# Kernel tuning notes

Hardware: AMD Instinct MI355X
Metric: run time of the kernel (lower is better)

## Reference

```python
import jax, jax.numpy as jnp
import numpy as np

E, D_MODEL, D_HIDDEN, TOK_PER_EXP = 64, 1024, 4096, 128


def setup_inputs() -> dict:
    key = jax.random.key(0)
    k1, k2, k3 = jax.random.split(key, 3)
    n_tokens = E * TOK_PER_EXP  # 8192
    inputs = jax.random.normal(k1, (n_tokens, D_MODEL), dtype=jnp.float32)
    # torch nn.Linear weights are [out_features, in_features]
    w1 = jax.random.normal(k2, (E, D_HIDDEN, D_MODEL), dtype=jnp.float32) * (1.0 / np.sqrt(D_MODEL))
    w2 = jax.random.normal(k3, (E, D_MODEL, D_HIDDEN), dtype=jnp.float32) * (1.0 / np.sqrt(D_HIDDEN))
    splits = np.full((E,), TOK_PER_EXP, dtype=np.int64)  # concrete host-side sizes, as in torch .tolist()
    return {"inputs": inputs, "w1": w1, "w2": w2, "splits": splits}


def reference(inputs, w1, w2, splits):
    # splits is a concrete (host) int array: chunk sizes along token dim, expert i uses splits[i % E].
    sizes = [int(s) for s in np.asarray(splits)]
    offsets = np.concatenate([[0], np.cumsum(sizes)])
    n_exp = w1.shape[0]
    outs = []
    for i, m in enumerate(sizes):  # loop over fixed expert list (structurally distinct weights)
        e = i % n_exp
        x = jax.lax.dynamic_slice_in_dim(inputs, int(offsets[i]), m, axis=0)  # [m, d_model]
        h = jax.nn.relu(x @ w1[e].T)          # [m, d_hidden]
        outs.append(h @ w2[e].T)              # [m, d_model]
    return jnp.concatenate(outs, axis=0)       # [N, d_model]
```

## Files before the change

kernel.cpp:

```cpp
#include <hip/hip_runtime.h>
#include <hip/hip_bf16.h>


typedef __attribute__((ext_vector_type(8))) short bf16x8;
typedef __attribute__((ext_vector_type(4))) float f32x4;
typedef __attribute__((ext_vector_type(4))) unsigned int u32x4;

#define N_EXPERTS 64
#define DM 1024
#define DH 4096
#define TOKS 128

__device__ __forceinline__ unsigned f2u(float f) {
    union { float f; unsigned u; } v; v.f = f; return v.u;
}
__device__ __forceinline__ unsigned short f2bf(float f) {
    return (unsigned short)((f2u(f) + 0x8000u) >> 16);
}
__device__ __forceinline__ unsigned pack2(float lo, float hi) {
    return ((f2u(lo) + 0x8000u) >> 16) | ((f2u(hi) + 0x8000u) & 0xFFFF0000u);
}

__global__ __launch_bounds__(256)
void cvt_bf16(const float* __restrict__ in, unsigned* __restrict__ outp, int n8) {
    int i = blockIdx.x * blockDim.x + threadIdx.x;
    if (i >= n8) return;
    const f32x4* p = (const f32x4*)in + (size_t)i * 2;
    f32x4 a = p[0], b = p[1];
    u32x4 o = { pack2(a[0], a[1]), pack2(a[2], a[3]),
                pack2(b[0], b[1]), pack2(b[2], b[3]) };
    *((u32x4*)outp + i) = o;
}

template<int N, int K, bool RELU_OUT_BF16>
__global__ __launch_bounds__(256, 2)
void moe_gemm(const unsigned short* __restrict__ Ab, const float* __restrict__ Bp,
              void* __restrict__ Cp, int nwg_per_xcd)
{
    constexpr int BK = 64;
    constexpr int NT = K / BK;
    constexpr int NTILES = N / 128;

    __shared__ unsigned short sA[2][128][BK];
    __shared__ unsigned short sB[2][128][BK];

    const int tid = threadIdx.x;
    const int bid = (blockIdx.x & 7) * nwg_per_xcd + (blockIdx.x >> 3);
    const int e   = bid / NTILES;
    const int nt  = bid % NTILES;

    const int lane = tid & 63;
    const int w    = tid >> 6;
    const int wr   = w >> 1;
    const int wc   = w & 1;
    const int lrow = lane & 15;
    const int kq   = lane >> 4;

    const int arow = tid >> 3;
    const int ac   = tid & 7;
    const int swz  = (arow >> 1) & 7;

    const unsigned short* aBase = Ab + (size_t)(e * TOKS + arow) * K + ac * 8;
    const float*          bBase = Bp + ((size_t)e * N + (size_t)nt * 128 + arow) * K + ac * 8;

    const int sl = (lrow >> 1) & 7;
    const int offk0 = ((kq + 0) ^ sl) * 8;
    const int offk1 = ((kq + 4) ^ sl) * 8;

    f32x4 acc[4][4];
    #pragma unroll
    for (int i = 0; i < 4; ++i)
        #pragma unroll
        for (int n = 0; n < 4; ++n)
            #pragma unroll
            for (int q = 0; q < 4; ++q) acc[i][n][q] = 0.f;

    struct Regs {
        u32x4 a[4];
        f32x4 b[8];
    };
    Regs r0, r1;

    auto LOAD = [&](int t, Regs& r) {
        #pragma unroll
        for (int j = 0; j < 4; ++j)
            r.a[j] = *(const u32x4*)(aBase + (size_t)j * 32 * K + t * BK);
        #pragma unroll
        for (int j = 0; j < 4; ++j) {
            const f32x4* p = (const f32x4*)(bBase + (size_t)j * 32 * K + t * BK);
            r.b[2 * j]     = __builtin_nontemporal_load(p);
            r.b[2 * j + 1] = __builtin_nontemporal_load(p + 1);
        }
    };

    auto WRITE = [&](int buf, Regs& r) {
        const int c8 = (ac ^ swz) * 8;
        #pragma unroll
        for (int j = 0; j < 4; ++j)
            *(u32x4*)&sA[buf][arow + j * 32][c8] = r.a[j];
        #pragma unroll
        for (int j = 0; j < 4; ++j) {
            f32x4 lo = r.b[2 * j], hi = r.b[2 * j + 1];
            u32x4 u = { pack2(lo[0], lo[1]), pack2(lo[2], lo[3]),
                        pack2(hi[0], hi[1]), pack2(hi[2], hi[3]) };
            *(u32x4*)&sB[buf][arow + j * 32][c8] = u;
        }
    };

    auto COMPUTE = [&](int buf) {
        #pragma unroll
        for (int kh = 0; kh < 2; ++kh) {
            const int off = kh ? offk1 : offk0;
            bf16x8 af[4], bfr[4];
            #pragma unroll
            for (int i = 0; i < 4; ++i)
                af[i] = *(const bf16x8*)&sA[buf][wr * 64 + i * 16 + lrow][off];
            #pragma unroll
            for (int n = 0; n < 4; ++n)
                bfr[n] = *(const bf16x8*)&sB[buf][wc * 64 + n * 16 + lrow][off];
            #pragma unroll
            for (int i = 0; i < 4; ++i)
                #pragma unroll
                for (int n = 0; n < 4; ++n)
                    acc[i][n] = __builtin_amdgcn_mfma_f32_16x16x32_bf16(af[i], bfr[n], acc[i][n], 0, 0, 0);
        }
    };

    LOAD(0, r0);
    LOAD(1, r1);
    WRITE(0, r0);
    asm volatile("s_waitcnt lgkmcnt(0)" ::: "memory");
    __builtin_amdgcn_s_barrier();

    for (int t = 0; t < NT; t += 2) {
        if (t + 2 < NT) LOAD(t + 2, r0);
        COMPUTE(0);
        if (t + 1 < NT) WRITE(1, r1);
        asm volatile("s_waitcnt lgkmcnt(0)" ::: "memory");
        __builtin_amdgcn_s_barrier();

        if (t + 3 < NT) LOAD(t + 3, r1);
        COMPUTE(1);
        if (t + 2 < NT) WRITE(0, r0);
        asm volatile("s_waitcnt lgkmcnt(0)" ::: "memory");
        __builtin_amdgcn_s_barrier();
    }

    const size_t crow0 = (size_t)e * TOKS;
    if constexpr (RELU_OUT_BF16) {
        unsigned short* C = (unsigned short*)Cp;
        #pragma unroll
        for (int i = 0; i < 4; ++i)
            #pragma unroll
            for (int n = 0; n < 4; ++n)
                #pragma unroll
                for (int q = 0; q < 4; ++q) {
                    const int row = wr * 64 + i * 16 + kq * 4 + q;
                    const int col = nt * 128 + wc * 64 + n * 16 + lrow;
                    C[(crow0 + row) * N + col] = f2bf(fmaxf(acc[i][n][q], 0.f));
                }
    } else {
        float* C = (float*)Cp;
        #pragma unroll
        for (int i = 0; i < 4; ++i)
            #pragma unroll
            for (int n = 0; n < 4; ++n)
                #pragma unroll
                for (int q = 0; q < 4; ++q) {
                    const int row = wr * 64 + i * 16 + kq * 4 + q;
                    const int col = nt * 128 + wc * 64 + n * 16 + lrow;
                    C[(crow0 + row) * N + col] = acc[i][n][q];
                }
    }
}

extern "C" void kernel_launch(void* const* d_in, const int* in_sizes, int n_in,
                              void* d_out, int out_size, void* d_ws, size_t ws_size,
                              hipStream_t stream) {
    const float* inputs = (const float*)d_in[0];
    const float* w1     = (const float*)d_in[1];
    const float* w2     = (const float*)d_in[2];

    unsigned short* h  = (unsigned short*)d_ws;
    unsigned short* xb = (unsigned short*)((char*)d_ws + (size_t)64 * 1024 * 1024);
    float* out = (float*)d_out;

    const int n8 = (TOKS * N_EXPERTS) * DM / 8;
    cvt_bf16<<<dim3(n8 / 256), dim3(256), 0, stream>>>(inputs, (unsigned*)xb, n8);

    moe_gemm<DH, DM, true><<<dim3(N_EXPERTS * (DH / 128)), dim3(256), 0, stream>>>(
        xb, w1, h, N_EXPERTS * (DH / 128) / 8);
    moe_gemm<DM, DH, false><<<dim3(N_EXPERTS * (DM / 128)), dim3(256), 0, stream>>>(
        h, w2, out, N_EXPERTS * (DM / 128) / 8);
}
```

Measured before the change: 521.1 us.

## Halve K tile to 32 and deepen register prefetch to three tiles

Cuts the K-tile from 64 to 32 and reorganises the global-to-register prefetch into four rotating register sets, so three K tiles of loads are in flight instead of two. Register use for staging stays about the same, and the LDS footprint per block halves. The aim is better hiding of global memory latency for the fp32 weight stream, which dominates this bandwidth-bound MoE GEMM. In exchange there are twice as many barriers per unit of K and fewer MFMAs between synchronisations, so the loop carries more sync overhead.

```diff
diff --git a/kernel.cpp b/kernel.cpp
--- a/kernel.cpp
+++ b/kernel.cpp
@@ -37,7 +37,7 @@
 void moe_gemm(const unsigned short* __restrict__ Ab, const float* __restrict__ Bp,
               void* __restrict__ Cp, int nwg_per_xcd)
 {
-    constexpr int BK = 64;
+    constexpr int BK = 32;
     constexpr int NT = K / BK;
     constexpr int NTILES = N / 128;
 
@@ -56,16 +56,14 @@
     const int lrow = lane & 15;
     const int kq   = lane >> 4;
 
-    const int arow = tid >> 3;
-    const int ac   = tid & 7;
-    const int swz  = (arow >> 1) & 7;
+    const int arow = tid >> 2;
+    const int ac   = tid & 3;
+    const int aswz = (arow >> 1) & 3;
 
     const unsigned short* aBase = Ab + (size_t)(e * TOKS + arow) * K + ac * 8;
     const float*          bBase = Bp + ((size_t)e * N + (size_t)nt * 128 + arow) * K + ac * 8;
 
-    const int sl = (lrow >> 1) & 7;
-    const int offk0 = ((kq + 0) ^ sl) * 8;
-    const int offk1 = ((kq + 4) ^ sl) * 8;
+    const int offk = ((kq ^ ((lrow >> 1) & 3))) * 8;
 
     f32x4 acc[4][4];
     #pragma unroll
@@ -75,73 +73,81 @@
             #pragma unroll
             for (int q = 0; q < 4; ++q) acc[i][n][q] = 0.f;
 
-    struct Regs {
-        u32x4 a[4];
-        f32x4 b[8];
-    };
-    Regs r0, r1;
-
-    auto LOAD = [&](int t, Regs& r) {
-        #pragma unroll
-        for (int j = 0; j < 4; ++j)
-            r.a[j] = *(const u32x4*)(aBase + (size_t)j * 32 * K + t * BK);
-        #pragma unroll
-        for (int j = 0; j < 4; ++j) {
-            const f32x4* p = (const f32x4*)(bBase + (size_t)j * 32 * K + t * BK);
-            r.b[2 * j]     = __builtin_nontemporal_load(p);
-            r.b[2 * j + 1] = __builtin_nontemporal_load(p + 1);
+    struct SetA { u32x4 a[2]; };
+    struct SetB { f32x4 b[4]; };
+    SetA sa0, sa1, sa2, sa3;
+    SetB sb0, sb1, sb2, sb3;
+
+    auto LOAD = [&](int t, SetA& A, SetB& B) {
+        #pragma unroll
+        for (int j = 0; j < 2; ++j)
+            A.a[j] = *(const u32x4*)(aBase + (size_t)j * 64 * K + t * BK);
+        #pragma unroll
+        for (int j = 0; j < 2; ++j) {
+            const f32x4* p = (const f32x4*)(bBase + (size_t)j * 64 * K + t * BK);
+            B.b[2 * j]     = __builtin_nontemporal_load(p);
+            B.b[2 * j + 1] = __builtin_nontemporal_load(p + 1);
         }
     };
 
-    auto WRITE = [&](int buf, Regs& r) {
-        const int c8 = (ac ^ swz) * 8;
-        #pragma unroll
-        for (int j = 0; j < 4; ++j)
-            *(u32x4*)&sA[buf][arow + j * 32][c8] = r.a[j];
-        #pragma unroll
-        for (int j = 0; j < 4; ++j) {
-            f32x4 lo = r.b[2 * j], hi = r.b[2 * j + 1];
+    auto WRITE = [&](int buf, SetA& A, SetB& B) {
+        const int c8 = (ac ^ aswz) * 8;
+        #pragma unroll
+        for (int j = 0; j < 2; ++j)
+            *(u32x4*)&sA[buf][arow + j * 64][c8] = A.a[j];
+        #pragma unroll
+        for (int j = 0; j < 2; ++j) {
+            f32x4 lo = B.b[2 * j], hi = B.b[2 * j + 1];
             u32x4 u = { pack2(lo[0], lo[1]), pack2(lo[2], lo[3]),
                         pack2(hi[0], hi[1]), pack2(hi[2], hi[3]) };
-            *(u32x4*)&sB[buf][arow + j * 32][c8] = u;
+            *(u32x4*)&sB[buf][arow + j * 64][c8] = u;
         }
     };
 
     auto COMPUTE = [&](int buf) {
-        #pragma unroll
-        for (int kh = 0; kh < 2; ++kh) {
-            const int off = kh ? offk1 : offk0;
-            bf16x8 af[4], bfr[4];
-            #pragma unroll
-            for (int i = 0; i < 4; ++i)
-                af[i] = *(const bf16x8*)&sA[buf][wr * 64 + i * 16 + lrow][off];
+        bf16x8 af[4], bfr[4];
+        #pragma unroll
+        for (int i = 0; i < 4; ++i)
+            af[i] = *(const bf16x8*)&sA[buf][wr * 64 + i * 16 + lrow][offk];
+        #pragma unroll
+        for (int n = 0; n < 4; ++n)
+            bfr[n] = *(const bf16x8*)&sB[buf][wc * 64 + n * 16 + lrow][offk];
+        #pragma unroll
+        for (int i = 0; i < 4; ++i)
             #pragma unroll
             for (int n = 0; n < 4; ++n)
-                bfr[n] = *(const bf16x8*)&sB[buf][wc * 64 + n * 16 + lrow][off];
-            #pragma unroll
-            for (int i = 0; i < 4; ++i)
-                #pragma unroll
-                for (int n = 0; n < 4; ++n)
-                    acc[i][n] = __builtin_amdgcn_mfma_f32_16x16x32_bf16(af[i], bfr[n], acc[i][n], 0, 0, 0);
-        }
+                acc[i][n] = __builtin_amdgcn_mfma_f32_16x16x32_bf16(af[i], bfr[n], acc[i][n], 0, 0, 0);
     };
 
-    LOAD(0, r0);
-    LOAD(1, r1);
-    WRITE(0, r0);
+    LOAD(0, sa0, sb0);
+    LOAD(1, sa1, sb1);
+    LOAD(2, sa2, sb2);
+    WRITE(0, sa0, sb0);
     asm volatile("s_waitcnt lgkmcnt(0)" ::: "memory");
     __builtin_amdgcn_s_barrier();
 
-    for (int t = 0; t < NT; t += 2) {
-        if (t + 2 < NT) LOAD(t + 2, r0);
+    for (int t = 0; t < NT; t += 4) {
+        if (t + 3 < NT) LOAD(t + 3, sa3, sb3);
         COMPUTE(0);
-        if (t + 1 < NT) WRITE(1, r1);
-        asm volatile("s_waitcnt lgkmcnt(0)" ::: "memory");
-        __builtin_amdgcn_s_barrier();
-
-        if (t + 3 < NT) LOAD(t + 3, r1);
+        WRITE(1, sa1, sb1);
+        asm volatile("s_waitcnt lgkmcnt(0)" ::: "memory");
+        __builtin_amdgcn_s_barrier();
+
+        if (t + 4 < NT) LOAD(t + 4, sa0, sb0);
         COMPUTE(1);
-        if (t + 2 < NT) WRITE(0, r0);
+        if (t + 2 < NT) WRITE(0, sa2, sb2);
+        asm volatile("s_waitcnt lgkmcnt(0)" ::: "memory");
+        __builtin_amdgcn_s_barrier();
+
+        if (t + 5 < NT) LOAD(t + 5, sa1, sb1);
+        COMPUTE(0);
+        if (t + 3 < NT) WRITE(1, sa3, sb3);
+        asm volatile("s_waitcnt lgkmcnt(0)" ::: "memory");
+        __builtin_amdgcn_s_barrier();
+
+        if (t + 6 < NT) LOAD(t + 6, sa2, sb2);
+        COMPUTE(1);
+        if (t + 4 < NT) WRITE(0, sa0, sb0);
         asm volatile("s_waitcnt lgkmcnt(0)" ::: "memory");
         __builtin_amdgcn_s_barrier();
     }
```

Result: no change. 529.1 us (+1.5%).

## Fuse both expert GEMMs into one persistent launch with per-expert completion counters

Applied to the files above, without the earlier changes.

Merges the two per-expert GEMM launches into a single kernel. The first 2048 blocks compute the ReLU hidden tiles and atomically bump a per-expert counter. The remaining 512 blocks spin on that counter until all 32 hidden tiles of their expert are done, then run the second GEMM. The counters are zeroed in the conversion kernel. This lets the second GEMM overlap with the tail of the first and removes a launch boundary. It relies on block dispatch order to avoid deadlock, and spinning blocks occupy CU slots while they wait.

```diff
diff --git a/kernel.cpp b/kernel.cpp
--- a/kernel.cpp
+++ b/kernel.cpp
@@ -22,8 +22,10 @@
 }
 
 __global__ __launch_bounds__(256)
-void cvt_bf16(const float* __restrict__ in, unsigned* __restrict__ outp, int n8) {
+void cvt_bf16(const float* __restrict__ in, unsigned* __restrict__ outp, int n8,
+              int* __restrict__ cnt) {
     int i = blockIdx.x * blockDim.x + threadIdx.x;
+    if (blockIdx.x == 0 && threadIdx.x < N_EXPERTS) cnt[threadIdx.x] = 0;
     if (i >= n8) return;
     const f32x4* p = (const f32x4*)in + (size_t)i * 2;
     f32x4 a = p[0], b = p[1];
@@ -33,21 +35,13 @@
 }
 
 template<int N, int K, bool RELU_OUT_BF16>
-__global__ __launch_bounds__(256, 2)
-void moe_gemm(const unsigned short* __restrict__ Ab, const float* __restrict__ Bp,
-              void* __restrict__ Cp, int nwg_per_xcd)
+__device__ __forceinline__
+void gemm_tile(const unsigned short* __restrict__ Ab, const float* __restrict__ Bp,
+               void* __restrict__ Cp, int e, int nt, int tid,
+               unsigned short (*sA)[128][64], unsigned short (*sB)[128][64])
 {
     constexpr int BK = 64;
     constexpr int NT = K / BK;
-    constexpr int NTILES = N / 128;
-
-    __shared__ unsigned short sA[2][128][BK];
-    __shared__ unsigned short sB[2][128][BK];
-
-    const int tid = threadIdx.x;
-    const int bid = (blockIdx.x & 7) * nwg_per_xcd + (blockIdx.x >> 3);
-    const int e   = bid / NTILES;
-    const int nt  = bid % NTILES;
 
     const int lane = tid & 63;
     const int w    = tid >> 6;
@@ -174,6 +168,43 @@
     }
 }
 
+__global__ __launch_bounds__(256, 2)
+void moe_fused(const unsigned short* __restrict__ xb, const float* __restrict__ w1,
+               const float* __restrict__ w2, unsigned short* __restrict__ h,
+               float* __restrict__ out, int* __restrict__ cnt)
+{
+    __shared__ unsigned short sA[2][128][64];
+    __shared__ unsigned short sB[2][128][64];
+
+    const int tid  = threadIdx.x;
+    const int slot = blockIdx.x;
+
+    if (slot < 2048) {
+        const int wid = (slot & 7) * 256 + (slot >> 3);
+        const int e   = wid >> 5;
+        const int nt  = wid & 31;
+        gemm_tile<DH, DM, true>(xb, w1, (void*)h, e, nt, tid, sA, sB);
+        __syncthreads();
+        if (tid == 0) {
+            __threadfence();
+            __hip_atomic_fetch_add(&cnt[e], 1, __ATOMIC_RELEASE,
+                                   __HIP_MEMORY_SCOPE_AGENT);
+        }
+    } else {
+        const int s2  = slot - 2048;
+        const int wid = (s2 & 7) * 64 + (s2 >> 3);
+        const int e   = wid >> 3;
+        const int nt  = wid & 7;
+        if (tid == 0) {
+            while (__hip_atomic_load(&cnt[e], __ATOMIC_ACQUIRE,
+                                     __HIP_MEMORY_SCOPE_AGENT) < 32)
+                __builtin_amdgcn_s_sleep(2);
+        }
+        __syncthreads();
+        gemm_tile<DM, DH, false>(h, w2, (void*)out, e, nt, tid, sA, sB);
+    }
+}
+
 extern "C" void kernel_launch(void* const* d_in, const int* in_sizes, int n_in,
                               void* d_out, int out_size, void* d_ws, size_t ws_size,
                               hipStream_t stream) {
@@ -183,13 +214,11 @@
 
     unsigned short* h  = (unsigned short*)d_ws;
     unsigned short* xb = (unsigned short*)((char*)d_ws + (size_t)64 * 1024 * 1024);
+    int* cnt = (int*)((char*)d_ws + (size_t)80 * 1024 * 1024);
     float* out = (float*)d_out;
 
     const int n8 = (TOKS * N_EXPERTS) * DM / 8;
-    cvt_bf16<<<dim3(n8 / 256), dim3(256), 0, stream>>>(inputs, (unsigned*)xb, n8);
-
-    moe_gemm<DH, DM, true><<<dim3(N_EXPERTS * (DH / 128)), dim3(256), 0, stream>>>(
-        xb, w1, h, N_EXPERTS * (DH / 128) / 8);
-    moe_gemm<DM, DH, false><<<dim3(N_EXPERTS * (DM / 128)), dim3(256), 0, stream>>>(
-        h, w2, out, N_EXPERTS * (DM / 128) / 8);
-}
+    cvt_bf16<<<dim3(n8 / 256), dim3(256), 0, stream>>>(inputs, (unsigned*)xb, n8, cnt);
+
+    moe_fused<<<dim3(2048 + 512), dim3(256), 0, stream>>>(xb, w1, w2, h, out, cnt);
+}
```

Result: slower. 693.6 us (+33.1%).

## Single-buffer LDS and registers to raise GEMM occupancy to four blocks

Applied to the files above, without the earlier changes.

Replaces the double-buffered LDS tiles and two register staging sets with a single buffer of each, and raises the launch bound to four workgroups per CU. The main loop now prefetches one tile ahead into registers and places a barrier before and after each LDS write. The goal is higher occupancy, so other resident waves hide global memory latency. In exchange it adds an extra barrier per K-step and drops intra-block overlap between writing the next tile and computing the current one, and it may force register spills under the tighter bound.

```diff
diff --git a/kernel.cpp b/kernel.cpp
--- a/kernel.cpp
+++ b/kernel.cpp
@@ -33,7 +33,7 @@
 }
 
 template<int N, int K, bool RELU_OUT_BF16>
-__global__ __launch_bounds__(256, 2)
+__global__ __launch_bounds__(256, 4)
 void moe_gemm(const unsigned short* __restrict__ Ab, const float* __restrict__ Bp,
               void* __restrict__ Cp, int nwg_per_xcd)
 {
@@ -41,8 +41,8 @@
     constexpr int NT = K / BK;
     constexpr int NTILES = N / 128;
 
-    __shared__ unsigned short sA[2][128][BK];
-    __shared__ unsigned short sB[2][128][BK];
+    __shared__ unsigned short sA[128][BK];
+    __shared__ unsigned short sB[128][BK];
 
     const int tid = threadIdx.x;
     const int bid = (blockIdx.x & 7) * nwg_per_xcd + (blockIdx.x >> 3);
@@ -79,9 +79,9 @@
         u32x4 a[4];
         f32x4 b[8];
     };
-    Regs r0, r1;
+    Regs r;
 
-    auto LOAD = [&](int t, Regs& r) {
+    auto LOAD = [&](int t) {
         #pragma unroll
         for (int j = 0; j < 4; ++j)
             r.a[j] = *(const u32x4*)(aBase + (size_t)j * 32 * K + t * BK);
@@ -93,31 +93,31 @@
         }
     };
 
-    auto WRITE = [&](int buf, Regs& r) {
+    auto WRITE = [&]() {
         const int c8 = (ac ^ swz) * 8;
         #pragma unroll
         for (int j = 0; j < 4; ++j)
-            *(u32x4*)&sA[buf][arow + j * 32][c8] = r.a[j];
+            *(u32x4*)&sA[arow + j * 32][c8] = r.a[j];
         #pragma unroll
         for (int j = 0; j < 4; ++j) {
             f32x4 lo = r.b[2 * j], hi = r.b[2 * j + 1];
             u32x4 u = { pack2(lo[0], lo[1]), pack2(lo[2], lo[3]),
                         pack2(hi[0], hi[1]), pack2(hi[2], hi[3]) };
-            *(u32x4*)&sB[buf][arow + j * 32][c8] = u;
+            *(u32x4*)&sB[arow + j * 32][c8] = u;
         }
     };
 
-    auto COMPUTE = [&](int buf) {
+    auto COMPUTE = [&]() {
         #pragma unroll
         for (int kh = 0; kh < 2; ++kh) {
             const int off = kh ? offk1 : offk0;
             bf16x8 af[4], bfr[4];
             #pragma unroll
             for (int i = 0; i < 4; ++i)
-                af[i] = *(const bf16x8*)&sA[buf][wr * 64 + i * 16 + lrow][off];
+                af[i] = *(const bf16x8*)&sA[wr * 64 + i * 16 + lrow][off];
             #pragma unroll
             for (int n = 0; n < 4; ++n)
-                bfr[n] = *(const bf16x8*)&sB[buf][wc * 64 + n * 16 + lrow][off];
+                bfr[n] = *(const bf16x8*)&sB[wc * 64 + n * 16 + lrow][off];
             #pragma unroll
             for (int i = 0; i < 4; ++i)
                 #pragma unroll
@@ -126,24 +126,20 @@
         }
     };
 
-    LOAD(0, r0);
-    LOAD(1, r1);
-    WRITE(0, r0);
+    LOAD(0);
+    WRITE();
     asm volatile("s_waitcnt lgkmcnt(0)" ::: "memory");
     __builtin_amdgcn_s_barrier();
 
-    for (int t = 0; t < NT; t += 2) {
-        if (t + 2 < NT) LOAD(t + 2, r0);
-        COMPUTE(0);
-        if (t + 1 < NT) WRITE(1, r1);
-        asm volatile("s_waitcnt lgkmcnt(0)" ::: "memory");
+    for (int t = 0; t < NT; ++t) {
+        if (t + 1 < NT) LOAD(t + 1);
+        COMPUTE();
         __builtin_amdgcn_s_barrier();
-
-        if (t + 3 < NT) LOAD(t + 3, r1);
-        COMPUTE(1);
-        if (t + 2 < NT) WRITE(0, r0);
-        asm volatile("s_waitcnt lgkmcnt(0)" ::: "memory");
-        __builtin_amdgcn_s_barrier();
+        if (t + 1 < NT) {
+            WRITE();
+            asm volatile("s_waitcnt lgkmcnt(0)" ::: "memory");
+            __builtin_amdgcn_s_barrier();
+        }
     }
 
     const size_t crow0 = (size_t)e * TOKS;
```

Result: slower. 645.9 us (+23.9%).
